# Kernel tuning notes

Measured on AMD Instinct MI355X. Metric: run time of the kernel, lower is better.

## Reference

```python
import jax, jax.numpy as jnp
import numpy as np

N, E, IN, H, OUT, G = 40000, 640000, 128, 128, 16, 64


def _sage(x, src, dst, Wl, Wr, b, n):
    # PyG SAGEConv (aggr='mean'): out = lin_l(mean_j x_j) + lin_r(x_i); bias in lin_l only
    msg = jnp.take(x, src, axis=0)                      # [E, d] gather
    s = jax.ops.segment_sum(msg, dst, num_segments=n)   # [N, d] scatter-add
    cnt = jax.ops.segment_sum(jnp.ones((src.shape[0], 1), x.dtype), dst, num_segments=n)
    agg = s / jnp.maximum(cnt, 1.0)                     # mean; 0 for isolated nodes
    return agg @ Wl.T + x @ Wr.T + b


def setup_inputs() -> dict:
    key = jax.random.key(0)
    ks = jax.random.split(key, 12)
    x = jax.random.normal(ks[0], (N, IN), jnp.float32)
    edge_index = jax.random.randint(ks[1], (2, E), 0, N, jnp.int64)
    batch = jnp.sort(jax.random.randint(ks[2], (N,), 0, G, jnp.int64))
    def lin(k, o, i):
        return jax.random.normal(k, (o, i), jnp.float32) / np.sqrt(i)
    return {
        "x": x, "edge_index": edge_index, "batch": batch,
        "W1l": lin(ks[3], H, IN), "W1r": lin(ks[4], H, IN), "b1": jnp.zeros((H,), jnp.float32),
        "W2l": lin(ks[5], H, H),  "W2r": lin(ks[6], H, H),  "b2": jnp.zeros((H,), jnp.float32),
        "W3l": lin(ks[7], H, H),  "W3r": lin(ks[8], H, H),  "b3": jnp.zeros((H,), jnp.float32),
        "Wfc": lin(ks[9], OUT, H), "bfc": jnp.zeros((OUT,), jnp.float32),
    }


def reference(x, edge_index, batch, W1l, W1r, b1, W2l, W2r, b2, W3l, W3r, b3, Wfc, bfc):
    src, dst = edge_index[0], edge_index[1]
    n = x.shape[0]
    h = jax.nn.relu(_sage(x, src, dst, W1l, W1r, b1, n))
    h = jax.nn.relu(_sage(h, src, dst, W2l, W2r, b2, n))
    h = jax.nn.relu(_sage(h, src, dst, W3l, W3r, b3, n))
    # global_mean_pool over graph ids
    s = jax.ops.segment_sum(h, batch, num_segments=G)
    cnt = jax.ops.segment_sum(jnp.ones((n, 1), h.dtype), batch, num_segments=G)
    pooled = s / jnp.maximum(cnt, 1.0)                  # [G, H]
    return pooled @ Wfc.T + bfc                          # [G, OUT]
```

## Files before the change

### kernel.cpp

```cpp
#include <hip/hip_runtime.h>

static constexpr int D = 128;
static constexpr int PS = 32;

typedef __attribute__((ext_vector_type(8))) short short8;
typedef __attribute__((ext_vector_type(4))) float f32x4;

__device__ inline ushort f2bf(float f) {
  union { float f; unsigned u; } v; v.f = f;
  unsigned r = v.u + 0x7FFF + ((v.u >> 16) & 1);
  return (ushort)(r >> 16);
}
__device__ inline float bf2f_lo(unsigned p) {
  union { unsigned u; float f; } v; v.u = p << 16; return v.f;
}
__device__ inline float bf2f_hi(unsigned p) {
  union { unsigned u; float f; } v; v.u = p & 0xFFFF0000u; return v.f;
}

struct WPtrs { const float* s[6]; ushort* d[6]; };

__global__ __launch_bounds__(256) void k_zero(uint4* __restrict__ p, int n16) {
  int i = blockIdx.x * 256 + threadIdx.x;
  if (i < n16) p[i] = (uint4){0u, 0u, 0u, 0u};
}

__global__ __launch_bounds__(256) void k_prep(const float* __restrict__ x, ushort* __restrict__ xb, WPtrs p,
                                              const int* __restrict__ dst, int* __restrict__ hist,
                                              int n4x, int E) {
  int b = blockIdx.x, tid = threadIdx.x;
  int nxb = (n4x + 255) / 256;
  if (b < nxb) {
    int i = b * 256 + tid;
    if (i < n4x) {
      float4 v = *(const float4*)&x[i * 4];
      ushort4 o;
      o.x = f2bf(v.x); o.y = f2bf(v.y); o.z = f2bf(v.z); o.w = f2bf(v.w);
      *(ushort4*)&xb[i * 4] = o;
    }
  } else if (b < nxb + 96) {
    int idx = (b - nxb) * 256 + tid;
    int mat = idx >> 12;
    int off = (idx & 4095) * 4;
    float4 v = *(const float4*)&p.s[mat][off];
    ushort4 o;
    o.x = f2bf(v.x); o.y = f2bf(v.y); o.z = f2bf(v.z); o.w = f2bf(v.w);
    *(ushort4*)&p.d[mat][off] = o;
  } else {
    int e = (b - nxb - 96) * 256 + tid;
    if (e < E) atomicAdd(&hist[dst[e]], 1);
  }
}

__global__ __launch_bounds__(1024) void k_scan(const int* __restrict__ hist, int* __restrict__ offsets, int n) {
  __shared__ int wsum[16];
  int tid = threadIdx.x, lane = tid & 63, w = tid >> 6;
  int carry = 0;
  for (int base = 0; base < n; base += 8192) {
    int i0 = base + tid * 8;
    int v[8];
    #pragma unroll
    for (int j = 0; j < 8; ++j) { int i = i0 + j; v[j] = (i < n) ? hist[i] : 0; }
    int s = 0;
    #pragma unroll
    for (int j = 0; j < 8; ++j) { int t = v[j]; v[j] = s; s += t; }
    int x = s;
    #pragma unroll
    for (int off = 1; off < 64; off <<= 1) {
      int t = __shfl_up(x, off);
      if (lane >= off) x += t;
    }
    if (lane == 63) wsum[w] = x;
    __syncthreads();
    int wpre = 0, total = 0;
    #pragma unroll
    for (int k = 0; k < 16; ++k) { int t = wsum[k]; total += t; if (k < w) wpre += t; }
    int pre = carry + wpre + x - s;
    #pragma unroll
    for (int j = 0; j < 8; ++j) { int i = i0 + j; if (i < n) offsets[i] = pre + v[j]; }
    carry += total;
    __syncthreads();
  }
  if (tid == 0) offsets[n] = carry;
}

__global__ __launch_bounds__(256) void k_fill(const int* __restrict__ src, const int* __restrict__ dst,
                                              const int* __restrict__ offsets, int* __restrict__ cursor,
                                              int* __restrict__ ssrc, int E) {
  int e = blockIdx.x * 256 + threadIdx.x;
  if (e < E) {
    int d = dst[e];
    int pos = offsets[d] + atomicAdd(&cursor[d], 1);
    ssrc[pos] = src[e];
  }
}

__global__ __launch_bounds__(256) void k_aggregate_bf(const ushort* __restrict__ X, const int* __restrict__ offsets,
                                                      const int* __restrict__ ssrc, ushort* __restrict__ Agg, int n) {
  int wid = (blockIdx.x * 256 + threadIdx.x) >> 6;
  int lane = threadIdx.x & 63;
  if (wid >= n) return;
  int q = lane >> 4, r = lane & 15;
  int o0 = offsets[wid], deg = offsets[wid + 1] - o0;

  float acc[8];
  #pragma unroll
  for (int i = 0; i < 8; ++i) acc[i] = 0.f;

  for (int c0 = 0; c0 < deg; c0 += 64) {
    int cn = min(64, deg - c0);
    int myid = (lane < cn) ? ssrc[o0 + c0 + lane] : 0;
    for (int j = 0; j < cn; j += 16) {
      uint4 buf[4];
      #pragma unroll
      for (int t = 0; t < 4; ++t) {
        int e = j + t * 4 + q;
        buf[t] = (uint4){0u, 0u, 0u, 0u};
        if (e < cn) {
          int s = __shfl(myid, e);
          buf[t] = *(const uint4*)&X[(size_t)s * D + r * 8];
        }
      }
      #pragma unroll
      for (int t = 0; t < 4; ++t) {
        acc[0] += bf2f_lo(buf[t].x); acc[1] += bf2f_hi(buf[t].x);
        acc[2] += bf2f_lo(buf[t].y); acc[3] += bf2f_hi(buf[t].y);
        acc[4] += bf2f_lo(buf[t].z); acc[5] += bf2f_hi(buf[t].z);
        acc[6] += bf2f_lo(buf[t].w); acc[7] += bf2f_hi(buf[t].w);
      }
    }
  }
  #pragma unroll
  for (int i = 0; i < 8; ++i) {
    acc[i] += __shfl_xor(acc[i], 16);
    acc[i] += __shfl_xor(acc[i], 32);
  }
  if (q == 0) {
    float inv = 1.f / (float)max(deg, 1);
    uint4 o;
    o.x = (unsigned)f2bf(acc[0] * inv) | ((unsigned)f2bf(acc[1] * inv) << 16);
    o.y = (unsigned)f2bf(acc[2] * inv) | ((unsigned)f2bf(acc[3] * inv) << 16);
    o.z = (unsigned)f2bf(acc[4] * inv) | ((unsigned)f2bf(acc[5] * inv) << 16);
    o.w = (unsigned)f2bf(acc[6] * inv) | ((unsigned)f2bf(acc[7] * inv) << 16);
    *(uint4*)&Agg[(size_t)wid * D + r * 8] = o;
  }
}

__global__ __launch_bounds__(256) void k_gemm_mfma(const ushort* __restrict__ Abf, const ushort* __restrict__ Xbf,
                                                   const ushort* __restrict__ Wl, const ushort* __restrict__ Wr,
                                                   const float* __restrict__ bias, ushort* __restrict__ Out, int n) {
  int tid = threadIdx.x;
  int wave = tid >> 6, lane = tid & 63;
  int wm = wave >> 1, wn = wave & 1;
  int m_base = blockIdx.x * 64 + wm * 32;
  int n_base = wn * 64;
  int r = lane & 15, kg = lane >> 4;

  f32x4 acc[2][4];
  #pragma unroll
  for (int i = 0; i < 2; ++i)
    #pragma unroll
    for (int j = 0; j < 4; ++j) acc[i][j] = (f32x4){0.f, 0.f, 0.f, 0.f};

  const ushort* As[2] = {Abf, Xbf};
  const ushort* Ws[2] = {Wl, Wr};
  #pragma unroll
  for (int half = 0; half < 2; ++half) {
    const ushort* A = As[half];
    const ushort* W = Ws[half];
    #pragma unroll
    for (int k0 = 0; k0 < 128; k0 += 32) {
      int kk = k0 + kg * 8;
      short8 a[2], b[4];
      #pragma unroll
      for (int fm = 0; fm < 2; ++fm)
        a[fm] = *(const short8*)&A[(size_t)(m_base + fm * 16 + r) * D + kk];
      #pragma unroll
      for (int fn = 0; fn < 4; ++fn)
        b[fn] = *(const short8*)&W[(size_t)(n_base + fn * 16 + r) * D + kk];
      #pragma unroll
      for (int fm = 0; fm < 2; ++fm)
        #pragma unroll
        for (int fn = 0; fn < 4; ++fn)
          acc[fm][fn] = __builtin_amdgcn_mfma_f32_16x16x32_bf16(a[fm], b[fn], acc[fm][fn], 0, 0, 0);
    }
  }
  #pragma unroll
  for (int fn = 0; fn < 4; ++fn) {
    int j = n_base + fn * 16 + r;
    float bj = bias[j];
    #pragma unroll
    for (int fm = 0; fm < 2; ++fm) {
      #pragma unroll
      for (int p = 0; p < 4; ++p) {
        int node = m_base + fm * 16 + kg * 4 + p;
        float v = fmaxf(acc[fm][fn][p] + bj, 0.f);
        Out[(size_t)node * D + j] = f2bf(v);
      }
    }
  }
}

__global__ __launch_bounds__(256) void k_pool_partial(const ushort* __restrict__ H, const int* __restrict__ batch,
                                                      float* __restrict__ partial, int n) {
  __shared__ float wsums[4][128];
  int g = blockIdx.x / PS, s = blockIdx.x % PS;
  int tid = threadIdx.x, wave = tid >> 6, lane = tid & 63;
  int a = 0, b = n;
  while (a < b) { int m = (a + b) >> 1; if (batch[m] < g) a = m + 1; else b = m; }
  int lo = a;
  b = n;
  while (a < b) { int m = (a + b) >> 1; if (batch[m] < g + 1) a = m + 1; else b = m; }
  int hi = a;
  int len = hi - lo;
  int chunk = (len + PS - 1) / PS;
  int a0 = lo + s * chunk;
  int a1 = min(a0 + chunk, hi);
  float ax = 0.f, ay = 0.f;
  for (int node = a0 + wave; node < a1; node += 4) {
    unsigned v = *(const unsigned*)&H[(size_t)node * D + lane * 2];
    ax += bf2f_lo(v);
    ay += bf2f_hi(v);
  }
  wsums[wave][lane * 2] = ax;
  wsums[wave][lane * 2 + 1] = ay;
  __syncthreads();
  if (tid < 128) {
    float v = wsums[0][tid] + wsums[1][tid] + wsums[2][tid] + wsums[3][tid];
    partial[(size_t)blockIdx.x * 128 + tid] = v;
  }
}

__global__ __launch_bounds__(256) void k_pool_fc2(const float* __restrict__ partial, const int* __restrict__ batch,
                                                  const float* __restrict__ Wfc, const float* __restrict__ bfc,
                                                  float* __restrict__ out, int n, int OUT) {
  __shared__ float pooled[128];
  int g = blockIdx.x;
  int tid = threadIdx.x, lane = tid & 63;
  int a = 0, b = n;
  while (a < b) { int m = (a + b) >> 1; if (batch[m] < g) a = m + 1; else b = m; }
  int lo = a;
  b = n;
  while (a < b) { int m = (a + b) >> 1; if (batch[m] < g + 1) a = m + 1; else b = m; }
  int hi = a;
  float inv = 1.f / (float)max(hi - lo, 1);
  if (tid < 128) {
    float v = 0.f;
    #pragma unroll
    for (int s = 0; s < PS; ++s) v += partial[(size_t)(g * PS + s) * 128 + tid];
    pooled[tid] = v * inv;
  }
  __syncthreads();
  if (tid < 64) {
    float2 p = *(const float2*)&pooled[lane * 2];
    for (int o = 0; o < OUT; ++o) {
      float2 w = *(const float2*)&Wfc[o * D + lane * 2];
      float part = p.x * w.x + p.y * w.y;
      #pragma unroll
      for (int off = 32; off > 0; off >>= 1) part += __shfl_down(part, off);
      if (lane == 0) out[g * OUT + o] = part + bfc[o];
    }
  }
}

extern "C" void kernel_launch(void* const* d_in, const int* in_sizes, int n_in,
                              void* d_out, int out_size, void* d_ws, size_t ws_size,
                              hipStream_t stream) {
  const float* x   = (const float*)d_in[0];
  const int* ei    = (const int*)d_in[1];
  const int* batch = (const int*)d_in[2];
  const float* W1l = (const float*)d_in[3];
  const float* W1r = (const float*)d_in[4];
  const float* b1  = (const float*)d_in[5];
  const float* W2l = (const float*)d_in[6];
  const float* W2r = (const float*)d_in[7];
  const float* b2  = (const float*)d_in[8];
  const float* W3l = (const float*)d_in[9];
  const float* W3r = (const float*)d_in[10];
  const float* b3  = (const float*)d_in[11];
  const float* Wfc = (const float*)d_in[12];
  const float* bfc = (const float*)d_in[13];
  float* out = (float*)d_out;

  int N = in_sizes[0] / D;
  int E = in_sizes[1] / 2;
  int OUT = in_sizes[12] / D;
  int G = out_size / OUT;
  const int* src = ei;
  const int* dst = ei + E;

  ushort* xb  = (ushort*)d_ws;
  ushort* agg = xb + (size_t)N * D;
  ushort* h1  = agg + (size_t)N * D;
  ushort* h2  = h1 + (size_t)N * D;
  ushort* wb  = h2 + (size_t)N * D;
  int* ssrc   = (int*)(wb + 6 * 128 * 128);
  int* hist   = ssrc + E;
  int* cursor = hist + N;
  int* offsets = cursor + N;
  float* partial = (float*)(offsets + N + 2);

  ushort* wl1 = wb + 0 * 16384; ushort* wr1 = wb + 1 * 16384;
  ushort* wl2 = wb + 2 * 16384; ushort* wr2 = wb + 3 * 16384;
  ushort* wl3 = wb + 4 * 16384; ushort* wr3 = wb + 5 * 16384;

  WPtrs wp;
  wp.s[0] = W1l; wp.s[1] = W1r; wp.s[2] = W2l; wp.s[3] = W2r; wp.s[4] = W3l; wp.s[5] = W3r;
  wp.d[0] = wl1; wp.d[1] = wr1; wp.d[2] = wl2; wp.d[3] = wr2; wp.d[4] = wl3; wp.d[5] = wr3;

  int n16 = (2 * N * 4) / 16;
  k_zero<<<(n16 + 255) / 256, 256, 0, stream>>>((uint4*)hist, n16);

  int n4 = N * D / 4;
  int nxb = (n4 + 255) / 256;
  int eb = (E + 255) / 256;
  k_prep<<<nxb + 96 + eb, 256, 0, stream>>>(x, xb, wp, dst, hist, n4, E);
  k_scan<<<1, 1024, 0, stream>>>(hist, offsets, N);
  k_fill<<<eb, 256, 0, stream>>>(src, dst, offsets, cursor, ssrc, E);

  int ab = (N * 64 + 255) / 256;
  int gb = (N + 63) / 64;

  k_aggregate_bf<<<ab, 256, 0, stream>>>(xb, offsets, ssrc, agg, N);
  k_gemm_mfma<<<gb, 256, 0, stream>>>(agg, xb, wl1, wr1, b1, h1, N);

  k_aggregate_bf<<<ab, 256, 0, stream>>>(h1, offsets, ssrc, agg, N);
  k_gemm_mfma<<<gb, 256, 0, stream>>>(agg, h1, wl2, wr2, b2, h2, N);

  k_aggregate_bf<<<ab, 256, 0, stream>>>(h2, offsets, ssrc, agg, N);
  k_gemm_mfma<<<gb, 256, 0, stream>>>(agg, h2, wl3, wr3, b3, h1, N);

  k_pool_partial<<<G * PS, 256, 0, stream>>>(h1, batch, partial, N);
  k_pool_fc2<<<G, 256, 0, stream>>>(partial, batch, Wfc, bfc, out, N, OUT);
}
```

Measured before the change: 263.4 us.

## Split aggregation feature dimension into four 32-column slices across blocks

The mean-aggregation kernel now splits each node's 128 features into four 32-wide slices, each handled by a separate block, so every wave gathers 4-byte words instead of 16-byte vectors per lane. This raises the wave count fourfold and cuts per-thread registers, aiming for more memory-level parallelism on the irregular gather. In exchange, each neighbor row is fetched in four separate 64-byte pieces, the edge list and offsets are read four times, and the per-lane load width shrinks, which may reduce gather efficiency.

```diff
diff --git a/kernel.cpp b/kernel.cpp
--- a/kernel.cpp
+++ b/kernel.cpp
@@ -97,52 +97,40 @@
 
 __global__ __launch_bounds__(256) void k_aggregate_bf(const ushort* __restrict__ X, const int* __restrict__ offsets,
                                                       const int* __restrict__ ssrc, ushort* __restrict__ Agg, int n) {
-  int wid = (blockIdx.x * 256 + threadIdx.x) >> 6;
+  int s = blockIdx.x & 3;
+  int node = (blockIdx.x >> 2) * 4 + (threadIdx.x >> 6);
   int lane = threadIdx.x & 63;
-  if (wid >= n) return;
+  if (node >= n) return;
   int q = lane >> 4, r = lane & 15;
-  int o0 = offsets[wid], deg = offsets[wid + 1] - o0;
-
-  float acc[8];
-  #pragma unroll
-  for (int i = 0; i < 8; ++i) acc[i] = 0.f;
+  int o0 = offsets[node], deg = offsets[node + 1] - o0;
+
+  float a0 = 0.f, a1 = 0.f;
+  const ushort* Xs = X + s * 32;
 
   for (int c0 = 0; c0 < deg; c0 += 64) {
     int cn = min(64, deg - c0);
     int myid = (lane < cn) ? ssrc[o0 + c0 + lane] : 0;
     for (int j = 0; j < cn; j += 16) {
-      uint4 buf[4];
+      unsigned buf[4];
       #pragma unroll
       for (int t = 0; t < 4; ++t) {
         int e = j + t * 4 + q;
-        buf[t] = (uint4){0u, 0u, 0u, 0u};
+        buf[t] = 0u;
         if (e < cn) {
-          int s = __shfl(myid, e);
-          buf[t] = *(const uint4*)&X[(size_t)s * D + r * 8];
+          int sid = __shfl(myid, e);
+          buf[t] = *(const unsigned*)&Xs[(size_t)sid * D + r * 2];
         }
       }
       #pragma unroll
-      for (int t = 0; t < 4; ++t) {
-        acc[0] += bf2f_lo(buf[t].x); acc[1] += bf2f_hi(buf[t].x);
-        acc[2] += bf2f_lo(buf[t].y); acc[3] += bf2f_hi(buf[t].y);
-        acc[4] += bf2f_lo(buf[t].z); acc[5] += bf2f_hi(buf[t].z);
-        acc[6] += bf2f_lo(buf[t].w); acc[7] += bf2f_hi(buf[t].w);
-      }
-    }
-  }
-  #pragma unroll
-  for (int i = 0; i < 8; ++i) {
-    acc[i] += __shfl_xor(acc[i], 16);
-    acc[i] += __shfl_xor(acc[i], 32);
-  }
+      for (int t = 0; t < 4; ++t) { a0 += bf2f_lo(buf[t]); a1 += bf2f_hi(buf[t]); }
+    }
+  }
+  a0 += __shfl_xor(a0, 16); a0 += __shfl_xor(a0, 32);
+  a1 += __shfl_xor(a1, 16); a1 += __shfl_xor(a1, 32);
   if (q == 0) {
     float inv = 1.f / (float)max(deg, 1);
-    uint4 o;
-    o.x = (unsigned)f2bf(acc[0] * inv) | ((unsigned)f2bf(acc[1] * inv) << 16);
-    o.y = (unsigned)f2bf(acc[2] * inv) | ((unsigned)f2bf(acc[3] * inv) << 16);
-    o.z = (unsigned)f2bf(acc[4] * inv) | ((unsigned)f2bf(acc[5] * inv) << 16);
-    o.w = (unsigned)f2bf(acc[6] * inv) | ((unsigned)f2bf(acc[7] * inv) << 16);
-    *(uint4*)&Agg[(size_t)wid * D + r * 8] = o;
+    unsigned o = (unsigned)f2bf(a0 * inv) | ((unsigned)f2bf(a1 * inv) << 16);
+    *(unsigned*)&Agg[(size_t)node * D + s * 32 + r * 2] = o;
   }
 }
 
@@ -318,7 +306,7 @@
   k_scan<<<1, 1024, 0, stream>>>(hist, offsets, N);
   k_fill<<<eb, 256, 0, stream>>>(src, dst, offsets, cursor, ssrc, E);
 
-  int ab = (N * 64 + 255) / 256;
+  int ab = ((N + 3) / 4) * 4;
   int gb = (N + 63) / 64;
 
   k_aggregate_bf<<<ab, 256, 0, stream>>>(xb, offsets, ssrc, agg, N);
```

Result: slower. 369.6 us (+40.3%).

## Fuse global mean-pool into last GEMM epilogue and widen aggregate gather batches

Applied to the files above, without the earlier changes.

The partial-pool kernel is removed. The third-layer GEMM epilogue now accumulates the post-ReLU values straight into a zeroed per-graph buffer with atomics, using a wave reduction when all 32 rows belong to one graph. This saves a kernel launch and a re-read of the final hidden states, at the cost of float atomics and a non-deterministic summation order. Separately, the aggregation loop now issues 8 outstanding 16-byte gathers per lane instead of 4, to raise memory-level parallelism at the cost of more registers.

```diff
diff --git a/kernel.cpp b/kernel.cpp
--- a/kernel.cpp
+++ b/kernel.cpp
@@ -1,7 +1,6 @@
 #include <hip/hip_runtime.h>
 
 static constexpr int D = 128;
-static constexpr int PS = 32;
 
 typedef __attribute__((ext_vector_type(8))) short short8;
 typedef __attribute__((ext_vector_type(4))) float f32x4;
@@ -110,10 +109,10 @@
   for (int c0 = 0; c0 < deg; c0 += 64) {
     int cn = min(64, deg - c0);
     int myid = (lane < cn) ? ssrc[o0 + c0 + lane] : 0;
-    for (int j = 0; j < cn; j += 16) {
-      uint4 buf[4];
-      #pragma unroll
-      for (int t = 0; t < 4; ++t) {
+    for (int j = 0; j < cn; j += 32) {
+      uint4 buf[8];
+      #pragma unroll
+      for (int t = 0; t < 8; ++t) {
         int e = j + t * 4 + q;
         buf[t] = (uint4){0u, 0u, 0u, 0u};
         if (e < cn) {
@@ -122,7 +121,7 @@
         }
       }
       #pragma unroll
-      for (int t = 0; t < 4; ++t) {
+      for (int t = 0; t < 8; ++t) {
         acc[0] += bf2f_lo(buf[t].x); acc[1] += bf2f_hi(buf[t].x);
         acc[2] += bf2f_lo(buf[t].y); acc[3] += bf2f_hi(buf[t].y);
         acc[4] += bf2f_lo(buf[t].z); acc[5] += bf2f_hi(buf[t].z);
@@ -148,7 +147,8 @@
 
 __global__ __launch_bounds__(256) void k_gemm_mfma(const ushort* __restrict__ Abf, const ushort* __restrict__ Xbf,
                                                    const ushort* __restrict__ Wl, const ushort* __restrict__ Wr,
-                                                   const float* __restrict__ bias, ushort* __restrict__ Out, int n) {
+                                                   const float* __restrict__ bias, ushort* __restrict__ Out,
+                                                   float* __restrict__ pool, const int* __restrict__ batch, int n) {
   int tid = threadIdx.x;
   int wave = tid >> 6, lane = tid & 63;
   int wm = wave >> 1, wn = wave & 1;
@@ -185,6 +185,17 @@
           acc[fm][fn] = __builtin_amdgcn_mfma_f32_16x16x32_bf16(a[fm], b[fn], acc[fm][fn], 0, 0, 0);
     }
   }
+
+  bool dopool = (pool != nullptr);
+  bool fast = false;
+  int g0 = 0;
+  if (dopool) {
+    g0 = batch[min(m_base, n - 1)];
+    int g1 = batch[min(m_base + 31, n - 1)];
+    fast = (g0 == g1);
+  }
+  float vsum[4] = {0.f, 0.f, 0.f, 0.f};
+
   #pragma unroll
   for (int fn = 0; fn < 4; ++fn) {
     int j = n_base + fn * 16 + r;
@@ -194,44 +205,29 @@
       #pragma unroll
       for (int p = 0; p < 4; ++p) {
         int node = m_base + fm * 16 + kg * 4 + p;
-        float v = fmaxf(acc[fm][fn][p] + bj, 0.f);
-        Out[(size_t)node * D + j] = f2bf(v);
+        if (node < n) {
+          float v = fmaxf(acc[fm][fn][p] + bj, 0.f);
+          Out[(size_t)node * D + j] = f2bf(v);
+          if (dopool) {
+            if (fast) vsum[fn] += v;
+            else atomicAdd(&pool[(size_t)batch[node] * 128 + j], v);
+          }
+        }
       }
     }
   }
-}
-
-__global__ __launch_bounds__(256) void k_pool_partial(const ushort* __restrict__ H, const int* __restrict__ batch,
-                                                      float* __restrict__ partial, int n) {
-  __shared__ float wsums[4][128];
-  int g = blockIdx.x / PS, s = blockIdx.x % PS;
-  int tid = threadIdx.x, wave = tid >> 6, lane = tid & 63;
-  int a = 0, b = n;
-  while (a < b) { int m = (a + b) >> 1; if (batch[m] < g) a = m + 1; else b = m; }
-  int lo = a;
-  b = n;
-  while (a < b) { int m = (a + b) >> 1; if (batch[m] < g + 1) a = m + 1; else b = m; }
-  int hi = a;
-  int len = hi - lo;
-  int chunk = (len + PS - 1) / PS;
-  int a0 = lo + s * chunk;
-  int a1 = min(a0 + chunk, hi);
-  float ax = 0.f, ay = 0.f;
-  for (int node = a0 + wave; node < a1; node += 4) {
-    unsigned v = *(const unsigned*)&H[(size_t)node * D + lane * 2];
-    ax += bf2f_lo(v);
-    ay += bf2f_hi(v);
-  }
-  wsums[wave][lane * 2] = ax;
-  wsums[wave][lane * 2 + 1] = ay;
-  __syncthreads();
-  if (tid < 128) {
-    float v = wsums[0][tid] + wsums[1][tid] + wsums[2][tid] + wsums[3][tid];
-    partial[(size_t)blockIdx.x * 128 + tid] = v;
-  }
-}
-
-__global__ __launch_bounds__(256) void k_pool_fc2(const float* __restrict__ partial, const int* __restrict__ batch,
+  if (dopool && fast) {
+    #pragma unroll
+    for (int fn = 0; fn < 4; ++fn) {
+      float s = vsum[fn];
+      s += __shfl_xor(s, 16);
+      s += __shfl_xor(s, 32);
+      if (kg == 0) atomicAdd(&pool[(size_t)g0 * 128 + n_base + fn * 16 + r], s);
+    }
+  }
+}
+
+__global__ __launch_bounds__(256) void k_pool_fc2(const float* __restrict__ pool, const int* __restrict__ batch,
                                                   const float* __restrict__ Wfc, const float* __restrict__ bfc,
                                                   float* __restrict__ out, int n, int OUT) {
   __shared__ float pooled[128];
@@ -244,12 +240,7 @@
   while (a < b) { int m = (a + b) >> 1; if (batch[m] < g + 1) a = m + 1; else b = m; }
   int hi = a;
   float inv = 1.f / (float)max(hi - lo, 1);
-  if (tid < 128) {
-    float v = 0.f;
-    #pragma unroll
-    for (int s = 0; s < PS; ++s) v += partial[(size_t)(g * PS + s) * 128 + tid];
-    pooled[tid] = v * inv;
-  }
+  if (tid < 128) pooled[tid] = pool[(size_t)g * 128 + tid] * inv;
   __syncthreads();
   if (tid < 64) {
     float2 p = *(const float2*)&pooled[lane * 2];
@@ -297,8 +288,8 @@
   int* ssrc   = (int*)(wb + 6 * 128 * 128);
   int* hist   = ssrc + E;
   int* cursor = hist + N;
-  int* offsets = cursor + N;
-  float* partial = (float*)(offsets + N + 2);
+  float* pool = (float*)(cursor + N);
+  int* offsets = (int*)(pool + (size_t)G * 128);
 
   ushort* wl1 = wb + 0 * 16384; ushort* wr1 = wb + 1 * 16384;
   ushort* wl2 = wb + 2 * 16384; ushort* wr2 = wb + 3 * 16384;
@@ -308,7 +299,8 @@
   wp.s[0] = W1l; wp.s[1] = W1r; wp.s[2] = W2l; wp.s[3] = W2r; wp.s[4] = W3l; wp.s[5] = W3r;
   wp.d[0] = wl1; wp.d[1] = wr1; wp.d[2] = wl2; wp.d[3] = wr2; wp.d[4] = wl3; wp.d[5] = wr3;
 
-  int n16 = (2 * N * 4) / 16;
+  int nz = 2 * N + G * 128;
+  int n16 = (nz + 3) / 4;
   k_zero<<<(n16 + 255) / 256, 256, 0, stream>>>((uint4*)hist, n16);
 
   int n4 = N * D / 4;
@@ -322,14 +314,13 @@
   int gb = (N + 63) / 64;
 
   k_aggregate_bf<<<ab, 256, 0, stream>>>(xb, offsets, ssrc, agg, N);
-  k_gemm_mfma<<<gb, 256, 0, stream>>>(agg, xb, wl1, wr1, b1, h1, N);
+  k_gemm_mfma<<<gb, 256, 0, stream>>>(agg, xb, wl1, wr1, b1, h1, nullptr, batch, N);
 
   k_aggregate_bf<<<ab, 256, 0, stream>>>(h1, offsets, ssrc, agg, N);
-  k_gemm_mfma<<<gb, 256, 0, stream>>>(agg, h1, wl2, wr2, b2, h2, N);
+  k_gemm_mfma<<<gb, 256, 0, stream>>>(agg, h1, wl2, wr2, b2, h2, nullptr, batch, N);
 
   k_aggregate_bf<<<ab, 256, 0, stream>>>(h2, offsets, ssrc, agg, N);
-  k_gemm_mfma<<<gb, 256, 0, stream>>>(agg, h2, wl3, wr3, b3, h1, N);
-
-  k_pool_partial<<<G * PS, 256, 0, stream>>>(h1, batch, partial, N);
-  k_pool_fc2<<<G, 256, 0, stream>>>(partial, batch, Wfc, bfc, out, N, OUT);
-}
+  k_gemm_mfma<<<gb, 256, 0, stream>>>(agg, h2, wl3, wr3, b3, h1, pool, batch, N);
+
+  k_pool_fc2<<<G, 256, 0, stream>>>(pool, batch, Wfc, bfc, out, N, OUT);
+}
```

Measured after the change: 312.0 us. 18.5% more time.
